# Kernel tuning notes

Measured on AMD Instinct MI355X. Metric: run time of the kernel, lower is better.

## Reference

```python
import jax, jax.numpy as jnp
import numpy as np

B, K, U, P, H, L = 4096, 512, 3, 5, 128, 32
N_SUB = 10
RATE_LO, RATE_HI = 0.01, 3.0


def setup_inputs() -> dict:
    key = jax.random.key(0)
    ks = jax.random.split(key, 8)
    f32 = jnp.float32
    return {
        "y0": jax.random.uniform(ks[0], (B, P), dtype=f32),
        "u_seq": jax.random.uniform(ks[1], (B, K, U), dtype=f32),
        "dt_seq": jax.random.uniform(ks[2], (B, K), dtype=f32),
        "lift_W": jax.random.normal(ks[3], (L, U + P), dtype=f32) * 0.1,
        "lift_b": jnp.zeros((L,), f32),
        "W_ih": jax.random.normal(ks[4], (3 * H, L), dtype=f32) * 0.1,
        "W_hh": jax.random.normal(ks[5], (3 * H, H), dtype=f32) * 0.1,
        "b_ih": jnp.zeros((3 * H,), f32),
        "b_hh": jnp.zeros((3 * H,), f32),
        "head_W": jax.random.normal(ks[6], (8, H), dtype=f32) * 0.1,
        "head_b": jnp.zeros((8,), f32),
        "u_to_x_jump": jax.random.uniform(ks[7], (U, P), dtype=f32) * 0.1,
    }


def _rhs(y, theta):
    # y: (B,5) [A,D,G,J,M], theta: (B,8) [kf1..kf4, kr1..kr4]
    A, D, G, J, M = (y[..., i] for i in range(5))
    kf1, kf2, kf3, kf4, kr1, kr2, kr3, kr4 = (theta[..., i] for i in range(8))
    dA = -kf1 * A + kr1 * D
    dD = kf1 * A - kr1 * D - kf2 * D + kr2 * G
    dG = kf2 * D - kr2 * G - kf3 * G + kr3 * J
    dJ = kf3 * G - kr3 * J - kf4 * J + kr4 * M
    dM = kf4 * J - kr4 * M
    return jnp.stack([dA, dD, dG, dJ, dM], axis=-1)


def _rk4_step(y, dt, theta):
    # y: (B,5), dt: (B,1), theta: (B,8)
    k1 = _rhs(y, theta)
    k2 = _rhs(y + 0.5 * dt * k1, theta)
    k3 = _rhs(y + 0.5 * dt * k2, theta)
    k4 = _rhs(y + dt * k3, theta)
    y_next = y + dt / 6.0 * (k1 + 2.0 * k2 + 2.0 * k3 + k4)
    return jnp.maximum(y_next, 0.0)  # clamp_min(0)


def reference(y0, u_seq, dt_seq, lift_W, lift_b, W_ih, W_hh, b_ih, b_hh,
              head_W, head_b, u_to_x_jump):
    Bd = y0.shape[0]

    def step(carry, xs):
        y_prev, h = carry
        u_k, dt_k = xs  # (B,U), (B,)
        # lift on [u_k, detached y_prev]
        feat = jnp.concatenate([u_k, jax.lax.stop_gradient(y_prev)], axis=-1)
        x = jax.nn.silu(feat @ lift_W.T + lift_b)
        # single-layer GRU cell (torch gate order: r, z, n)
        gi = x @ W_ih.T + b_ih    # (B,3H)
        gh = h @ W_hh.T + b_hh    # (B,3H)
        r = jax.nn.sigmoid(gi[:, :H] + gh[:, :H])
        z = jax.nn.sigmoid(gi[:, H:2 * H] + gh[:, H:2 * H])
        n = jnp.tanh(gi[:, 2 * H:] + r * gh[:, 2 * H:])
        h_new = (1.0 - z) * n + z * h
        raw = h_new @ head_W.T + head_b
        theta = RATE_LO + (RATE_HI - RATE_LO) * jax.nn.sigmoid(raw)
        # input-induced state jump, then RK4 with N_SUB substeps
        y = y_prev + u_k @ u_to_x_jump
        hsub = (dt_k / float(N_SUB))[:, None]
        for _ in range(N_SUB):  # small fixed substep count
            y = _rk4_step(y, hsub, theta)
        return (y, h_new), (y, theta)

    y_prev0 = y0 + 0.01
    h0 = jnp.zeros((Bd, H), y0.dtype)
    xs = (jnp.swapaxes(u_seq, 0, 1), dt_seq.T)  # (K,B,U), (K,B)
    _, (y_out, theta_out) = jax.lax.scan(step, (y_prev0, h0), xs)
    y_out = jnp.swapaxes(y_out, 0, 1)          # (B,K,5)
    theta_out = jnp.swapaxes(theta_out, 0, 1)  # (B,K,8)
    return y_out, theta_out
```

## Files before the change

### kernel.cpp

```cpp
#include <hip/hip_runtime.h>


#define KSTEPS 512
#define NTH 512

typedef short s16x8 __attribute__((ext_vector_type(8)));
typedef short s16x4 __attribute__((ext_vector_type(4)));
typedef float f32x4 __attribute__((ext_vector_type(4)));

__device__ __forceinline__ unsigned short f2bf(float f) {
  union { float f; unsigned u; } v; v.f = f;
  unsigned r = v.u + 0x7FFFu + ((v.u >> 16) & 1u);
  return (unsigned short)(r >> 16);
}
__device__ __forceinline__ unsigned cvt2bf(float lo, float hi) {
  unsigned r;
  asm("v_cvt_pk_bf16_f32 %0, %1, %2" : "=v"(r) : "v"(lo), "v"(hi));
  return r;
}
__device__ __forceinline__ float ex2(float x) {
#if __has_builtin(__builtin_amdgcn_exp2f)
  return __builtin_amdgcn_exp2f(x);
#else
  return exp2f(x);
#endif
}
__device__ __forceinline__ float rcp_(float x) {
#if __has_builtin(__builtin_amdgcn_rcpf)
  return __builtin_amdgcn_rcpf(x);
#else
  return 1.0f / x;
#endif
}
__device__ __forceinline__ float sigm(float x) {
  return rcp_(1.0f + ex2(-1.44269504088896f * x));
}
__device__ __forceinline__ float tanh_(float x) {
  return fmaf(2.0f, rcp_(1.0f + ex2(-2.88539008177793f * x)), -1.0f);
}
__device__ __forceinline__ f32x4 splat4(float v) { f32x4 r = {v, v, v, v}; return r; }
__device__ __forceinline__ f32x4 MFMA(s16x8 a, s16x8 b, f32x4 c) {
  return __builtin_amdgcn_mfma_f32_16x16x32_bf16(a, b, c, 0, 0, 0);
}
__device__ __forceinline__ s16x8 bfrag_g(const float* __restrict__ src8) {
  s16x8 r;
#pragma unroll
  for (int j = 0; j < 8; ++j) r[j] = (short)f2bf(src8[j]);
  return r;
}

__global__ __launch_bounds__(NTH, 2) void rnn_scan_kernel(
    const float* __restrict__ y0, const float* __restrict__ u_seq,
    const float* __restrict__ dt_seq, const float* __restrict__ lift_W,
    const float* __restrict__ lift_b, const float* __restrict__ W_ih,
    const float* __restrict__ W_hh, const float* __restrict__ b_ih,
    const float* __restrict__ b_hh, const float* __restrict__ head_W,
    const float* __restrict__ head_b, const float* __restrict__ jumpW,
    float* __restrict__ y_out, float* __restrict__ th_out) {
  __shared__ __align__(16) unsigned short s_Ah[4096];
  __shared__ __align__(16) unsigned short s_Ax[1024];
  __shared__ __align__(16) float s_thr[2][16][8];
  __shared__ __align__(16) float s_yr[2][16][8];

  const int tid = threadIdx.x;
  const int w = tid >> 6;
  const int lane = tid & 63;
  const int quad = lane >> 4;
  const int col = lane & 15;
  const int r0 = blockIdx.x << 4;

  s16x8 zf;
#pragma unroll
  for (int j = 0; j < 8; ++j) zf[j] = 0;

  s16x8 bih_r = bfrag_g(&W_ih[(w * 16 + col) * 32 + quad * 8]);
  s16x8 bih_z = bfrag_g(&W_ih[((8 + w) * 16 + col) * 32 + quad * 8]);
  s16x8 bih_n = bfrag_g(&W_ih[((16 + w) * 16 + col) * 32 + quad * 8]);
  s16x8 bhh_r[4], bhh_z[4], bhh_n[4], bhdF[4], bhdR[4];
#pragma unroll
  for (int s = 0; s < 4; ++s) {
    bhh_r[s] = bfrag_g(&W_hh[(w * 16 + col) * 128 + s * 32 + quad * 8]);
    bhh_z[s] = bfrag_g(&W_hh[((8 + w) * 16 + col) * 128 + s * 32 + quad * 8]);
    bhh_n[s] = bfrag_g(&W_hh[((16 + w) * 16 + col) * 128 + s * 32 + quad * 8]);
    bhdF[s] = bfrag_g(&head_W[(col & 3) * 128 + s * 32 + quad * 8]);
    bhdR[s] = bfrag_g(&head_W[(4 + (col & 3)) * 128 + s * 32 + quad * 8]);
  }
  s16x8 blft0 = (quad == 0) ? bfrag_g(&lift_W[col * 8]) : zf;
  s16x8 blft1 = (quad == 0) ? bfrag_g(&lift_W[(16 + col) * 8]) : zf;

  f32x4 brz_r, brz_z, bn_iv, bn_hv, lbv0, lbv1, hbF, hbR;
#pragma unroll
  for (int i = 0; i < 4; ++i) {
    int g = w * 16 + quad * 4 + i;
    brz_r[i] = b_ih[g] + b_hh[g];
    brz_z[i] = b_ih[128 + g] + b_hh[128 + g];
    bn_iv[i] = b_ih[256 + g];
    bn_hv[i] = b_hh[256 + g];
    lbv0[i] = lift_b[quad * 4 + i];
    lbv1[i] = lift_b[16 + quad * 4 + i];
    hbF[i] = head_b[i];
    hbR[i] = head_b[4 + i];
  }
  float J[15];
#pragma unroll
  for (int i = 0; i < 15; ++i) J[i] = jumpW[i];

  const int hwoff = (((w >> 1) * 64 + ((w & 1) * 2 + (quad >> 1)) * 16 + col) << 4) +
                    ((quad & 1) << 3);
  const int xw0 = ((((quad >> 1)) * 16 + col) << 4) + ((quad & 1) << 3);
  const int xw1 = (((2 + (quad >> 1)) * 16 + col) << 4) + ((quad & 1) << 3);

  f32x4 ar = brz_r, az = brz_z, angi = bn_iv, angh = bn_hv;
  f32x4 h_reg = splat4(0.0f);
  float y[5] = {0.f, 0.f, 0.f, 0.f, 0.f};
  float uc0 = 0.f, uc1 = 0.f, uc2 = 0.f, dtc = 0.f;
  float un0 = 0.f, un1 = 0.f, un2 = 0.f, dtn = 0.f;

  if (w == 7) {
    if (quad == 0) {
      const float* yp = &y0[(r0 + col) * 5];
#pragma unroll
      for (int i = 0; i < 5; ++i) y[i] = yp[i] + 0.01f;
      const float* up = &u_seq[((size_t)(r0 + col) * KSTEPS) * 3];
      uc0 = up[0]; uc1 = up[1]; uc2 = up[2];
      dtc = dt_seq[(size_t)(r0 + col) * KSTEPS];
    }
    s16x8 af = zf;
    if (quad == 0) {
      union { s16x8 v; unsigned u[4]; } afu;
      afu.u[0] = cvt2bf(uc0, uc1);
      afu.u[1] = cvt2bf(uc2, y[0]);
      afu.u[2] = cvt2bf(y[1], y[2]);
      afu.u[3] = cvt2bf(y[3], y[4]);
      af = afu.v;
    }
    f32x4 x0 = MFMA(blft0, af, lbv0);
    f32x4 x1 = MFMA(blft1, af, lbv1);
    f32x4 s0, s1;
#pragma unroll
    for (int i = 0; i < 4; ++i) {
      float v0 = x0[i]; s0[i] = v0 * sigm(v0);
      float v1 = x1[i]; s1[i] = v1 * sigm(v1);
    }
    uint2 xp0, xp1;
    xp0.x = cvt2bf(s0[0], s0[1]); xp0.y = cvt2bf(s0[2], s0[3]);
    xp1.x = cvt2bf(s1[0], s1[1]); xp1.y = cvt2bf(s1[2], s1[3]);
    *(uint2*)((char*)s_Ax + xw0) = xp0;
    *(uint2*)((char*)s_Ax + xw1) = xp1;
  }
  __syncthreads();

#pragma unroll 1
  for (int k = 0; k < KSTEPS; ++k) {
    {
      s16x8 xf = *(const s16x8*)((const char*)s_Ax + lane * 16);
      ar = MFMA(bih_r, xf, ar);
      az = MFMA(bih_z, xf, az);
      angi = MFMA(bih_n, xf, angi);
    }
    if (w == 7 && quad == 0) {
      int kn = (k + 1 < KSTEPS) ? k + 1 : KSTEPS - 1;
      const float* up = &u_seq[((size_t)(r0 + col) * KSTEPS + kn) * 3];
      un0 = up[0]; un1 = up[1]; un2 = up[2];
      dtn = dt_seq[(size_t)(r0 + col) * KSTEPS + kn];
    }
    {
      f32x4 hf;
#pragma unroll
      for (int i = 0; i < 4; ++i) {
        float r = sigm(ar[i]);
        float z = sigm(az[i]);
        float n = tanh_(fmaf(r, angh[i], angi[i]));
        float hn = fmaf(z, h_reg[i] - n, n);
        h_reg[i] = hn;
        hf[i] = hn;
      }
      uint2 hp;
      hp.x = cvt2bf(hf[0], hf[1]);
      hp.y = cvt2bf(hf[2], hf[3]);
      *(uint2*)((char*)s_Ah + hwoff) = hp;
    }
    ar = brz_r; az = brz_z; angi = bn_iv; angh = bn_hv;
    __syncthreads();

    s16x8 ah[4];
#pragma unroll
    for (int s = 0; s < 4; ++s)
      ah[s] = *(const s16x8*)((const char*)s_Ah + (s * 64 + lane) * 16);

    if (w == 7) {
      __builtin_amdgcn_s_setprio(1);
      f32x4 hdF0 = MFMA(bhdF[0], ah[0], hbF);
      f32x4 hdF1 = MFMA(bhdF[1], ah[1], splat4(0.0f));
      f32x4 hdR0 = MFMA(bhdR[0], ah[0], hbR);
      f32x4 hdR1 = MFMA(bhdR[1], ah[1], splat4(0.0f));
      hdF0 = MFMA(bhdF[2], ah[2], hdF0);
      hdF1 = MFMA(bhdF[3], ah[3], hdF1);
      hdR0 = MFMA(bhdR[2], ah[2], hdR0);
      hdR1 = MFMA(bhdR[3], ah[3], hdR1);
#pragma unroll
      for (int s = 0; s < 4; ++s) {
        ar = MFMA(bhh_r[s], ah[s], ar);
        az = MFMA(bhh_z[s], ah[s], az);
        angh = MFMA(bhh_n[s], ah[s], angh);
      }
      f32x4 hdF = hdF0 + hdF1;
      f32x4 hdR = hdR0 + hdR1;
      f32x4 tvF, tvR;
#pragma unroll
      for (int i = 0; i < 4; ++i) {
        tvF[i] = fmaf(2.99f, sigm(hdF[i]), 0.01f);
        tvR[i] = fmaf(2.99f, sigm(hdR[i]), 0.01f);
      }
      const int slot = k & 1;
      if (quad == 0) {
        *(f32x4*)&s_thr[slot][col][0] = tvF;
        *(f32x4*)&s_thr[slot][col][4] = tvR;
      }
      const float F0 = tvF[0], F1 = tvF[1], F2 = tvF[2], F3 = tvF[3];
      const float R0 = tvR[0], R1 = tvR[1], R2 = tvR[2], R3 = tvR[3];
#pragma unroll
      for (int i = 0; i < 5; ++i)
        y[i] += uc0 * J[i] + uc1 * J[5 + i] + uc2 * J[10 + i];
      const float hs = dtc * 0.1f;

      const float TD0 = -(F0 + R0), TD1 = -(F1 + R1), TD2 = -(F2 + R2), TD3 = -(F3 + R3);
      const float c4 = 0.25f * hs, c3 = hs * (1.0f / 3.0f), c2 = 0.5f * hs;
      const float d30 = fmaf(c4, TD0, 1.f), d31 = fmaf(c4, TD1, 1.f);
      const float d32 = fmaf(c4, TD2, 1.f), d33 = fmaf(c4, TD3, 1.f);
      const float l31 = c4 * F1, l32 = c4 * F2, l33 = c4 * F3;
      const float u30 = c4 * R0, u31 = c4 * R1, u32 = c4 * R2;
      const float w300 = fmaf(TD0, d30, R0 * l31);
      const float w301 = fmaf(TD0, u30, R0 * d31);
      const float w302 = R0 * u31;
      const float w310 = fmaf(F1, d30, TD1 * l31);
      const float w311 = fmaf(F1, u30, fmaf(TD1, d31, R1 * l32));
      const float w312 = fmaf(TD1, u31, R1 * d32);
      const float w313 = R1 * u32;
      const float w320 = F2 * l31;
      const float w321 = fmaf(F2, d31, TD2 * l32);
      const float w322 = fmaf(F2, u31, fmaf(TD2, d32, R2 * l33));
      const float w323 = fmaf(TD2, u32, R2 * d33);
      const float w331 = F3 * l32;
      const float w332 = fmaf(F3, d32, TD3 * l33);
      const float w333 = fmaf(F3, u32, TD3 * d33);
      const float e20 = fmaf(c3, w300, 1.f), e21 = fmaf(c3, w311, 1.f);
      const float e22 = fmaf(c3, w322, 1.f), e23 = fmaf(c3, w333, 1.f);
      const float a201 = c3 * w301, a202 = c3 * w302;
      const float a210 = c3 * w310, a212 = c3 * w312, a213 = c3 * w313;
      const float a220 = c3 * w320, a221 = c3 * w321, a223 = c3 * w323;
      const float a231 = c3 * w331, a232 = c3 * w332;
      const float w200 = fmaf(TD0, e20, R0 * a210);
      const float w201 = fmaf(TD0, a201, R0 * e21);
      const float w202 = fmaf(TD0, a202, R0 * a212);
      const float w203 = R0 * a213;
      const float w210 = fmaf(F1, e20, fmaf(TD1, a210, R1 * a220));
      const float w211 = fmaf(F1, a201, fmaf(TD1, e21, R1 * a221));
      const float w212 = fmaf(F1, a202, fmaf(TD1, a212, R1 * e22));
      const float w213 = fmaf(TD1, a213, R1 * a223);
      const float w220 = fmaf(F2, a210, TD2 * a220);
      const float w221 = fmaf(F2, e21, fmaf(TD2, a221, R2 * a231));
      const float w222 = fmaf(F2, a212, fmaf(TD2, e22, R2 * a232));
      const float w223 = fmaf(F2, a213, fmaf(TD2, a223, R2 * e23));
      const float w230 = F3 * a220;
      const float w231 = fmaf(F3, a221, TD3 * a231);
      const float w232 = fmaf(F3, e22, TD3 * a232);
      const float w233 = fmaf(F3, a223, TD3 * e23);
      const float z100 = fmaf(c2, w200, 1.f), z101 = c2 * w201, z102 = c2 * w202, z103 = c2 * w203;
      const float z110 = c2 * w210, z111 = fmaf(c2, w211, 1.f), z112 = c2 * w212, z113 = c2 * w213;
      const float z120 = c2 * w220, z121 = c2 * w221, z122 = fmaf(c2, w222, 1.f), z123 = c2 * w223;
      const float z130 = c2 * w230, z131 = c2 * w231, z132 = c2 * w232, z133 = fmaf(c2, w233, 1.f);
      const float FH0 = hs * F0, FH1 = hs * F1, FH2 = hs * F2, FH3 = hs * F3;
      const float RH0 = hs * R0, RH1 = hs * R1, RH2 = hs * R2, RH3 = hs * R3;
      const float pc00 = z100 * FH0;
      const float pc01 = fmaf(z101, FH1, -(z100 * RH0));
      const float pc02 = fmaf(z102, FH2, -(z101 * RH1));
      const float pc03 = fmaf(z103, FH3, -(z102 * RH2));
      const float pc04 = -(z103 * RH3);
      const float pc10 = z110 * FH0;
      const float pc11 = fmaf(z111, FH1, -(z110 * RH0));
      const float pc12 = fmaf(z112, FH2, -(z111 * RH1));
      const float pc13 = fmaf(z113, FH3, -(z112 * RH2));
      const float pc14 = -(z113 * RH3);
      const float pc20 = z120 * FH0;
      const float pc21 = fmaf(z121, FH1, -(z120 * RH0));
      const float pc22 = fmaf(z122, FH2, -(z121 * RH1));
      const float pc23 = fmaf(z123, FH3, -(z122 * RH2));
      const float pc24 = -(z123 * RH3);
      const float pc30 = z130 * FH0;
      const float pc31 = fmaf(z131, FH1, -(z130 * RH0));
      const float pc32 = fmaf(z132, FH2, -(z131 * RH1));
      const float pc33 = fmaf(z133, FH3, -(z132 * RH2));
      const float pc34 = -(z133 * RH3);
      float Mm[5][5];
      Mm[0][0] = 1.0f - pc00; Mm[0][1] = -pc01; Mm[0][2] = -pc02; Mm[0][3] = -pc03; Mm[0][4] = -pc04;
      Mm[1][0] = pc00 - pc10; Mm[1][1] = 1.0f + (pc01 - pc11); Mm[1][2] = pc02 - pc12;
      Mm[1][3] = pc03 - pc13; Mm[1][4] = pc04 - pc14;
      Mm[2][0] = pc10 - pc20; Mm[2][1] = pc11 - pc21; Mm[2][2] = 1.0f + (pc12 - pc22);
      Mm[2][3] = pc13 - pc23; Mm[2][4] = pc14 - pc24;
      Mm[3][0] = pc20 - pc30; Mm[3][1] = pc21 - pc31; Mm[3][2] = pc22 - pc32;
      Mm[3][3] = 1.0f + (pc23 - pc33); Mm[3][4] = pc24 - pc34;
      Mm[4][0] = pc30; Mm[4][1] = pc31; Mm[4][2] = pc32; Mm[4][3] = pc33;
      Mm[4][4] = 1.0f + pc34;
      float M2[5][5];
#pragma unroll
      for (int i = 0; i < 5; ++i) {
#pragma unroll
        for (int j = 0; j < 5; ++j) {
          float acc = Mm[i][0] * Mm[0][j];
#pragma unroll
          for (int l = 1; l < 5; ++l) acc = fmaf(Mm[i][l], Mm[l][j], acc);
          M2[i][j] = acc;
        }
      }
#pragma unroll
      for (int ss = 0; ss < 5; ++ss) {
        float n[5];
#pragma unroll
        for (int i = 0; i < 5; ++i) {
          float acc = M2[i][0] * y[0];
#pragma unroll
          for (int j = 1; j < 5; ++j) acc = fmaf(M2[i][j], y[j], acc);
          n[i] = acc;
        }
#pragma unroll
        for (int i = 0; i < 5; ++i) y[i] = fmaxf(n[i], 0.0f);
      }
      if (quad == 0) {
        *(f32x4*)&s_yr[slot][col][0] = *(const f32x4*)&y[0];
        s_yr[slot][col][4] = y[4];
      }
      if (k + 1 < KSTEPS) {
        s16x8 af = zf;
        if (quad == 0) {
          union { s16x8 v; unsigned u[4]; } afu;
          afu.u[0] = cvt2bf(un0, un1);
          afu.u[1] = cvt2bf(un2, y[0]);
          afu.u[2] = cvt2bf(y[1], y[2]);
          afu.u[3] = cvt2bf(y[3], y[4]);
          af = afu.v;
        }
        f32x4 x0 = MFMA(blft0, af, lbv0);
        f32x4 x1 = MFMA(blft1, af, lbv1);
        f32x4 s0, s1;
#pragma unroll
        for (int i = 0; i < 4; ++i) {
          float v0 = x0[i]; s0[i] = v0 * sigm(v0);
          float v1 = x1[i]; s1[i] = v1 * sigm(v1);
        }
        uint2 xp0, xp1;
        xp0.x = cvt2bf(s0[0], s0[1]); xp0.y = cvt2bf(s0[2], s0[3]);
        xp1.x = cvt2bf(s1[0], s1[1]); xp1.y = cvt2bf(s1[2], s1[3]);
        *(uint2*)((char*)s_Ax + xw0) = xp0;
        *(uint2*)((char*)s_Ax + xw1) = xp1;
      }
      uc0 = un0; uc1 = un1; uc2 = un2; dtc = dtn;
      __builtin_amdgcn_s_setprio(0);
    } else {
#pragma unroll
      for (int s = 0; s < 4; ++s) {
        ar = MFMA(bhh_r[s], ah[s], ar);
        az = MFMA(bhh_z[s], ah[s], az);
        angh = MFMA(bhh_n[s], ah[s], angh);
      }
      if (w == 0 && k > 0) {
        const int km = k - 1, slot = km & 1;
#pragma unroll
        for (int rep = 0; rep < 2; ++rep) {
          int idx = lane + rep * 64;
          int row = idx >> 3, c = idx & 7;
          th_out[((size_t)(r0 + row) * KSTEPS + km) * 8 + c] = s_thr[slot][row][c];
        }
        {
          int idx = lane;
          int row = idx / 5, c = idx - row * 5;
          y_out[((size_t)(r0 + row) * KSTEPS + km) * 5 + c] = s_yr[slot][row][c];
        }
        if (lane < 16) {
          int idx = 64 + lane;
          int row = idx / 5, c = idx - row * 5;
          y_out[((size_t)(r0 + row) * KSTEPS + km) * 5 + c] = s_yr[slot][row][c];
        }
      }
    }
    __syncthreads();
  }

  if (w == 0) {
    const int km = KSTEPS - 1, slot = km & 1;
#pragma unroll
    for (int rep = 0; rep < 2; ++rep) {
      int idx = lane + rep * 64;
      int row = idx >> 3, c = idx & 7;
      th_out[((size_t)(r0 + row) * KSTEPS + km) * 8 + c] = s_thr[slot][row][c];
    }
    {
      int idx = lane;
      int row = idx / 5, c = idx - row * 5;
      y_out[((size_t)(r0 + row) * KSTEPS + km) * 5 + c] = s_yr[slot][row][c];
    }
    if (lane < 16) {
      int idx = 64 + lane;
      int row = idx / 5, c = idx - row * 5;
      y_out[((size_t)(r0 + row) * KSTEPS + km) * 5 + c] = s_yr[slot][row][c];
    }
  }
}

extern "C" void kernel_launch(void* const* d_in, const int* in_sizes, int n_in,
                              void* d_out, int out_size, void* d_ws, size_t ws_size,
                              hipStream_t stream) {
  const float* y0 = (const float*)d_in[0];
  const float* u_seq = (const float*)d_in[1];
  const float* dt_seq = (const float*)d_in[2];
  const float* lift_W = (const float*)d_in[3];
  const float* lift_b = (const float*)d_in[4];
  const float* W_ih = (const float*)d_in[5];
  const float* W_hh = (const float*)d_in[6];
  const float* b_ih = (const float*)d_in[7];
  const float* b_hh = (const float*)d_in[8];
  const float* head_W = (const float*)d_in[9];
  const float* head_b = (const float*)d_in[10];
  const float* jumpW = (const float*)d_in[11];

  float* y_out = (float*)d_out;
  float* th_out = y_out + (size_t)4096 * 512 * 5;

  rnn_scan_kernel<<<dim3(256), dim3(NTH), 0, stream>>>(
      y0, u_seq, dt_seq, lift_W, lift_b, W_ih, W_hh, b_ih, b_hh, head_W,
      head_b, jumpW, y_out, th_out);
}
```

Baseline: 1.102 ms.

## Replace dense 5x5 RK4 matrix squaring with flux-space Neumann-style series and prefetch inputs via LDS

The per-step ODE propagation previously built a full 5x5 step matrix, squared it, and applied it five times with a clamp after each application. It now computes a 4x4 flux-space propagator G, iterates it nine times on the flux vector, accumulates the results and applies the conservative update once, with no intermediate clamp. Loading of u_seq and dt_seq moves off the critical wave 7 into wave 1, which fills a triple-buffered shared-memory ring two steps ahead. The aim is to shorten the serial critical path of wave 7. The risk is that dropping the per-substep max(0) changes results whenever states would go negative.

```diff
diff --git a/kernel.cpp b/kernel.cpp
--- a/kernel.cpp
+++ b/kernel.cpp
@@ -61,6 +61,7 @@
   __shared__ __align__(16) unsigned short s_Ax[1024];
   __shared__ __align__(16) float s_thr[2][16][8];
   __shared__ __align__(16) float s_yr[2][16][8];
+  __shared__ __align__(16) float s_ur[3][16][4];
 
   const int tid = threadIdx.x;
   const int w = tid >> 6;
@@ -113,17 +114,25 @@
   f32x4 ar = brz_r, az = brz_z, angi = bn_iv, angh = bn_hv;
   f32x4 h_reg = splat4(0.0f);
   float y[5] = {0.f, 0.f, 0.f, 0.f, 0.f};
-  float uc0 = 0.f, uc1 = 0.f, uc2 = 0.f, dtc = 0.f;
-  float un0 = 0.f, un1 = 0.f, un2 = 0.f, dtn = 0.f;
-
+
+  if (w == 1 && lane < 16) {
+#pragma unroll
+    for (int pk = 0; pk < 2; ++pk) {
+      const float* up = &u_seq[((size_t)(r0 + lane) * KSTEPS + pk) * 3];
+      f32x4 uv;
+      uv[0] = up[0]; uv[1] = up[1]; uv[2] = up[2];
+      uv[3] = dt_seq[(size_t)(r0 + lane) * KSTEPS + pk];
+      *(f32x4*)&s_ur[pk][lane][0] = uv;
+    }
+  }
   if (w == 7) {
+    float uc0 = 0.f, uc1 = 0.f, uc2 = 0.f;
     if (quad == 0) {
       const float* yp = &y0[(r0 + col) * 5];
 #pragma unroll
       for (int i = 0; i < 5; ++i) y[i] = yp[i] + 0.01f;
       const float* up = &u_seq[((size_t)(r0 + col) * KSTEPS) * 3];
       uc0 = up[0]; uc1 = up[1]; uc2 = up[2];
-      dtc = dt_seq[(size_t)(r0 + col) * KSTEPS];
     }
     s16x8 af = zf;
     if (quad == 0) {
@@ -150,6 +159,8 @@
   }
   __syncthreads();
 
+  int sA = 0, sB = 1, sC = 2;
+
 #pragma unroll 1
   for (int k = 0; k < KSTEPS; ++k) {
     {
@@ -158,12 +169,6 @@
       az = MFMA(bih_z, xf, az);
       angi = MFMA(bih_n, xf, angi);
     }
-    if (w == 7 && quad == 0) {
-      int kn = (k + 1 < KSTEPS) ? k + 1 : KSTEPS - 1;
-      const float* up = &u_seq[((size_t)(r0 + col) * KSTEPS + kn) * 3];
-      un0 = up[0]; un1 = up[1]; un2 = up[2];
-      dtn = dt_seq[(size_t)(r0 + col) * KSTEPS + kn];
-    }
     {
       f32x4 hf;
 #pragma unroll
@@ -190,6 +195,8 @@
 
     if (w == 7) {
       __builtin_amdgcn_s_setprio(1);
+      f32x4 urk = *(const f32x4*)&s_ur[sA][col][0];
+      f32x4 urk1 = *(const f32x4*)&s_ur[sB][col][0];
       f32x4 hdF0 = MFMA(bhdF[0], ah[0], hbF);
       f32x4 hdF1 = MFMA(bhdF[1], ah[1], splat4(0.0f));
       f32x4 hdR0 = MFMA(bhdR[0], ah[0], hbR);
@@ -221,8 +228,8 @@
       const float R0 = tvR[0], R1 = tvR[1], R2 = tvR[2], R3 = tvR[3];
 #pragma unroll
       for (int i = 0; i < 5; ++i)
-        y[i] += uc0 * J[i] + uc1 * J[5 + i] + uc2 * J[10 + i];
-      const float hs = dtc * 0.1f;
+        y[i] += urk[0] * J[i] + urk[1] * J[5 + i] + urk[2] * J[10 + i];
+      const float hs = urk[3] * 0.1f;
 
       const float TD0 = -(F0 + R0), TD1 = -(F1 + R1), TD2 = -(F2 + R2), TD3 = -(F3 + R3);
       const float c4 = 0.25f * hs, c3 = hs * (1.0f / 3.0f), c2 = 0.5f * hs;
@@ -270,62 +277,51 @@
       const float z110 = c2 * w210, z111 = fmaf(c2, w211, 1.f), z112 = c2 * w212, z113 = c2 * w213;
       const float z120 = c2 * w220, z121 = c2 * w221, z122 = fmaf(c2, w222, 1.f), z123 = c2 * w223;
       const float z130 = c2 * w230, z131 = c2 * w231, z132 = c2 * w232, z133 = fmaf(c2, w233, 1.f);
+      const float q00 = fmaf(TD0, z100, R0 * z110);
+      const float q01 = fmaf(TD0, z101, R0 * z111);
+      const float q02 = fmaf(TD0, z102, R0 * z112);
+      const float q03 = fmaf(TD0, z103, R0 * z113);
+      const float q10 = fmaf(F1, z100, fmaf(TD1, z110, R1 * z120));
+      const float q11 = fmaf(F1, z101, fmaf(TD1, z111, R1 * z121));
+      const float q12 = fmaf(F1, z102, fmaf(TD1, z112, R1 * z122));
+      const float q13 = fmaf(F1, z103, fmaf(TD1, z113, R1 * z123));
+      const float q20 = fmaf(F2, z110, fmaf(TD2, z120, R2 * z130));
+      const float q21 = fmaf(F2, z111, fmaf(TD2, z121, R2 * z131));
+      const float q22 = fmaf(F2, z112, fmaf(TD2, z122, R2 * z132));
+      const float q23 = fmaf(F2, z113, fmaf(TD2, z123, R2 * z133));
+      const float q30 = fmaf(F3, z120, TD3 * z130);
+      const float q31 = fmaf(F3, z121, TD3 * z131);
+      const float q32 = fmaf(F3, z122, TD3 * z132);
+      const float q33 = fmaf(F3, z123, TD3 * z133);
+      const float g00 = fmaf(hs, q00, 1.f), g01 = hs * q01, g02 = hs * q02, g03 = hs * q03;
+      const float g10 = hs * q10, g11 = fmaf(hs, q11, 1.f), g12 = hs * q12, g13 = hs * q13;
+      const float g20 = hs * q20, g21 = hs * q21, g22 = fmaf(hs, q22, 1.f), g23 = hs * q23;
+      const float g30 = hs * q30, g31 = hs * q31, g32 = hs * q32, g33 = fmaf(hs, q33, 1.f);
       const float FH0 = hs * F0, FH1 = hs * F1, FH2 = hs * F2, FH3 = hs * F3;
       const float RH0 = hs * R0, RH1 = hs * R1, RH2 = hs * R2, RH3 = hs * R3;
-      const float pc00 = z100 * FH0;
-      const float pc01 = fmaf(z101, FH1, -(z100 * RH0));
-      const float pc02 = fmaf(z102, FH2, -(z101 * RH1));
-      const float pc03 = fmaf(z103, FH3, -(z102 * RH2));
-      const float pc04 = -(z103 * RH3);
-      const float pc10 = z110 * FH0;
-      const float pc11 = fmaf(z111, FH1, -(z110 * RH0));
-      const float pc12 = fmaf(z112, FH2, -(z111 * RH1));
-      const float pc13 = fmaf(z113, FH3, -(z112 * RH2));
-      const float pc14 = -(z113 * RH3);
-      const float pc20 = z120 * FH0;
-      const float pc21 = fmaf(z121, FH1, -(z120 * RH0));
-      const float pc22 = fmaf(z122, FH2, -(z121 * RH1));
-      const float pc23 = fmaf(z123, FH3, -(z122 * RH2));
-      const float pc24 = -(z123 * RH3);
-      const float pc30 = z130 * FH0;
-      const float pc31 = fmaf(z131, FH1, -(z130 * RH0));
-      const float pc32 = fmaf(z132, FH2, -(z131 * RH1));
-      const float pc33 = fmaf(z133, FH3, -(z132 * RH2));
-      const float pc34 = -(z133 * RH3);
-      float Mm[5][5];
-      Mm[0][0] = 1.0f - pc00; Mm[0][1] = -pc01; Mm[0][2] = -pc02; Mm[0][3] = -pc03; Mm[0][4] = -pc04;
-      Mm[1][0] = pc00 - pc10; Mm[1][1] = 1.0f + (pc01 - pc11); Mm[1][2] = pc02 - pc12;
-      Mm[1][3] = pc03 - pc13; Mm[1][4] = pc04 - pc14;
-      Mm[2][0] = pc10 - pc20; Mm[2][1] = pc11 - pc21; Mm[2][2] = 1.0f + (pc12 - pc22);
-      Mm[2][3] = pc13 - pc23; Mm[2][4] = pc14 - pc24;
-      Mm[3][0] = pc20 - pc30; Mm[3][1] = pc21 - pc31; Mm[3][2] = pc22 - pc32;
-      Mm[3][3] = 1.0f + (pc23 - pc33); Mm[3][4] = pc24 - pc34;
-      Mm[4][0] = pc30; Mm[4][1] = pc31; Mm[4][2] = pc32; Mm[4][3] = pc33;
-      Mm[4][4] = 1.0f + pc34;
-      float M2[5][5];
-#pragma unroll
-      for (int i = 0; i < 5; ++i) {
-#pragma unroll
-        for (int j = 0; j < 5; ++j) {
-          float acc = Mm[i][0] * Mm[0][j];
-#pragma unroll
-          for (int l = 1; l < 5; ++l) acc = fmaf(Mm[i][l], Mm[l][j], acc);
-          M2[i][j] = acc;
-        }
-      }
-#pragma unroll
-      for (int ss = 0; ss < 5; ++ss) {
-        float n[5];
-#pragma unroll
-        for (int i = 0; i < 5; ++i) {
-          float acc = M2[i][0] * y[0];
-#pragma unroll
-          for (int j = 1; j < 5; ++j) acc = fmaf(M2[i][j], y[j], acc);
-          n[i] = acc;
-        }
-#pragma unroll
-        for (int i = 0; i < 5; ++i) y[i] = fmaxf(n[i], 0.0f);
-      }
+      float w0 = fmaf(FH0, y[0], -(RH0 * y[1]));
+      float w1 = fmaf(FH1, y[1], -(RH1 * y[2]));
+      float w2 = fmaf(FH2, y[2], -(RH2 * y[3]));
+      float w3 = fmaf(FH3, y[3], -(RH3 * y[4]));
+      float a0 = w0, a1 = w1, a2 = w2, a3 = w3;
+#pragma unroll
+      for (int ss = 0; ss < 9; ++ss) {
+        float t0 = fmaf(g00, w0, fmaf(g01, w1, fmaf(g02, w2, g03 * w3)));
+        float t1 = fmaf(g10, w0, fmaf(g11, w1, fmaf(g12, w2, g13 * w3)));
+        float t2 = fmaf(g20, w0, fmaf(g21, w1, fmaf(g22, w2, g23 * w3)));
+        float t3 = fmaf(g30, w0, fmaf(g31, w1, fmaf(g32, w2, g33 * w3)));
+        w0 = t0; w1 = t1; w2 = t2; w3 = t3;
+        a0 += t0; a1 += t1; a2 += t2; a3 += t3;
+      }
+      const float s0f = fmaf(z100, a0, fmaf(z101, a1, fmaf(z102, a2, z103 * a3)));
+      const float s1f = fmaf(z110, a0, fmaf(z111, a1, fmaf(z112, a2, z113 * a3)));
+      const float s2f = fmaf(z120, a0, fmaf(z121, a1, fmaf(z122, a2, z123 * a3)));
+      const float s3f = fmaf(z130, a0, fmaf(z131, a1, fmaf(z132, a2, z133 * a3)));
+      y[0] -= s0f;
+      y[1] += s0f - s1f;
+      y[2] += s1f - s2f;
+      y[3] += s2f - s3f;
+      y[4] += s3f;
       if (quad == 0) {
         *(f32x4*)&s_yr[slot][col][0] = *(const f32x4*)&y[0];
         s_yr[slot][col][4] = y[4];
@@ -334,8 +330,8 @@
         s16x8 af = zf;
         if (quad == 0) {
           union { s16x8 v; unsigned u[4]; } afu;
-          afu.u[0] = cvt2bf(un0, un1);
-          afu.u[1] = cvt2bf(un2, y[0]);
+          afu.u[0] = cvt2bf(urk1[0], urk1[1]);
+          afu.u[1] = cvt2bf(urk1[2], y[0]);
           afu.u[2] = cvt2bf(y[1], y[2]);
           afu.u[3] = cvt2bf(y[3], y[4]);
           af = afu.v;
@@ -354,7 +350,6 @@
         *(uint2*)((char*)s_Ax + xw0) = xp0;
         *(uint2*)((char*)s_Ax + xw1) = xp1;
       }
-      uc0 = un0; uc1 = un1; uc2 = un2; dtc = dtn;
       __builtin_amdgcn_s_setprio(0);
     } else {
 #pragma unroll
@@ -362,6 +357,14 @@
         ar = MFMA(bhh_r[s], ah[s], ar);
         az = MFMA(bhh_z[s], ah[s], az);
         angh = MFMA(bhh_n[s], ah[s], angh);
+      }
+      if (w == 1 && lane < 16) {
+        int kn2 = (k + 2 < KSTEPS) ? k + 2 : KSTEPS - 1;
+        const float* up = &u_seq[((size_t)(r0 + lane) * KSTEPS + kn2) * 3];
+        f32x4 uv;
+        uv[0] = up[0]; uv[1] = up[1]; uv[2] = up[2];
+        uv[3] = dt_seq[(size_t)(r0 + lane) * KSTEPS + kn2];
+        *(f32x4*)&s_ur[sC][lane][0] = uv;
       }
       if (w == 0 && k > 0) {
         const int km = k - 1, slot = km & 1;
@@ -384,6 +387,7 @@
       }
     }
     __syncthreads();
+    int st = sA; sA = sB; sB = sC; sC = st;
   }
 
   if (w == 0) {
```

New measurement: 1.024 ms. -7.1%, faster.
